# Kernel tuning notes

Hardware: AMD Instinct MI355X
Metric: run time of the kernel (lower is better)

## Reference

```python
import jax, jax.numpy as jnp
import numpy as np

N_NODES = 50000
N_EDGES = 1_600_000
T = 2
F_IN = 128
F_OUT = 128


def setup_inputs() -> dict:
    key = jax.random.key(0)
    k1, k2, k3, k4, k5, k6 = jax.random.split(key, 6)
    node_features = jax.random.normal(k1, (N_NODES, T, F_IN), dtype=jnp.float32)
    edge_weights = jax.random.uniform(k2, (T, N_EDGES), dtype=jnp.float32)
    src = jax.random.randint(k3, (N_EDGES,), 0, N_NODES, dtype=jnp.int32)
    dst = jax.random.randint(k4, (N_EDGES,), 0, N_NODES, dtype=jnp.int32)
    W = jax.random.normal(k5, (F_OUT, F_IN), dtype=jnp.float32) / np.sqrt(F_IN)
    b = jax.random.normal(k6, (F_OUT,), dtype=jnp.float32) * 0.01
    return {"node_features": node_features, "edge_weights": edge_weights,
            "src": src, "dst": dst, "W": W, "b": b}


def reference(node_features, edge_weights, src, dst, W, b):
    # DGL: graph.edata['e'] = edge_weights.t().unsqueeze(-1)  -> [E, T, 1]
    w = jnp.transpose(edge_weights)[:, :, None]          # [E, T, 1]
    # u_mul_e: gather src node features, scale by edge weight -> [E, T, F]
    msg = node_features[src] * w
    # sum aggregation at destination nodes -> [N, T, F]
    h = jax.ops.segment_sum(msg, dst, num_segments=node_features.shape[0])
    # Linear(in_features, out_features) with bias
    return jnp.einsum('ntf,of->nto', h, W) + b
```

## Files before the change

kernel.cpp:

```cpp
#include <hip/hip_runtime.h>
#include <hip/hip_bf16.h>
#include <hip/hip_fp16.h>


#define TBLOCK 256
#define CAP 64
#define NGRP 8
#define GSH 5
#define GSZ (1 << GSH)
#define NQ 1563
#define BCAP 224
#define APB 1536

typedef _Float16 half8 __attribute__((ext_vector_type(8)));
typedef float    f32x4 __attribute__((ext_vector_type(4)));
typedef float    float4_v __attribute__((ext_vector_type(4)));

__global__ void __launch_bounds__(TBLOCK)
prep_kernel(const float* __restrict__ W, _Float16* __restrict__ Wfrag,
            int* __restrict__ qcnt, int qtotal) {
    int i = blockIdx.x * TBLOCK + threadIdx.x;
    if (i < 128 * 128) {
        int j  = i & 7;
        int r  = (i >> 3) & 15;
        int q  = i >> 7;
        int kg = q & 3;
        int s  = (q >> 2) & 3;
        int c  = q >> 4;
        Wfrag[i] = (_Float16)W[(size_t)(c * 16 + r) * 128 + s * 32 + kg * 8 + j];
    }
    if (i < qtotal) qcnt[i] = 0;
}

__device__ __forceinline__ void do_append(
        const int* __restrict__ src, const int* __restrict__ dst,
        const float* __restrict__ ew, int* __restrict__ qcnt,
        unsigned long long* __restrict__ buckets, int E, int ablk) {
    const int g = ablk & (NGRP - 1);
    int* qc = qcnt + (size_t)g * NQ;
    unsigned long long* bk = buckets + (size_t)g * NQ * BCAP;

    const int idx = ablk * TBLOCK + (int)threadIdx.x;
    const int stride = APB * TBLOCK * 4;

    for (int e4 = idx * 4; e4 < E; e4 += stride) {
        if (e4 + 3 < E) {
            int4   d4  = *(const int4*)&dst[e4];
            int4   s4  = *(const int4*)&src[e4];
            float4 w04 = *(const float4*)&ew[e4];
            float4 w14 = *(const float4*)&ew[(size_t)E + e4];
            const int   dd[4] = {d4.x, d4.y, d4.z, d4.w};
            const int   ss[4] = {s4.x, s4.y, s4.z, s4.w};
            const float w0[4] = {w04.x, w04.y, w04.z, w04.w};
            const float w1[4] = {w14.x, w14.y, w14.z, w14.w};
            #pragma unroll
            for (int k = 0; k < 4; ++k) {
                int d = dd[k];
                int q = d >> GSH, dloc = d & (GSZ - 1);
                int pos = atomicAdd(&qc[q], 1);
                if (pos < BCAP) {
                    __half2 hw = __floats2half2_rn(w0[k], w1[k]);
                    bk[(size_t)q * BCAP + pos] =
                        (unsigned long long)(unsigned)(ss[k] | (dloc << 16)) |
                        ((unsigned long long)(*(unsigned*)&hw) << 32);
                }
            }
        } else {
            for (int e = e4; e < E; ++e) {
                int d = dst[e];
                int q = d >> GSH, dloc = d & (GSZ - 1);
                int pos = atomicAdd(&qc[q], 1);
                if (pos < BCAP) {
                    __half2 hw = __floats2half2_rn(ew[e], ew[(size_t)E + e]);
                    bk[(size_t)q * BCAP + pos] =
                        (unsigned long long)(unsigned)(src[e] | (dloc << 16)) |
                        ((unsigned long long)(*(unsigned*)&hw) << 32);
                }
            }
        }
    }
}

__device__ __forceinline__ void do_transform(
        const float* __restrict__ x, const _Float16* __restrict__ Wfrag,
        __half* __restrict__ y, int nrows, int blk) {
    const int tid = threadIdx.x;
    const int l   = tid & 63;
    const int wv  = tid >> 6;
    const int r15 = l & 15;
    const int kg  = l >> 4;
    const int row = blk * 64 + wv * 16 + r15;
    const bool ok = row < nrows;

    const float* xrow = x + (size_t)(ok ? row : 0) * 128;

    half8 xf[4];
    #pragma unroll
    for (int s = 0; s < 4; ++s) {
        float4 u0 = *(const float4*)&xrow[s * 32 + kg * 8];
        float4 u1 = *(const float4*)&xrow[s * 32 + kg * 8 + 4];
        half8 h;
        h[0] = (_Float16)u0.x; h[1] = (_Float16)u0.y;
        h[2] = (_Float16)u0.z; h[3] = (_Float16)u0.w;
        h[4] = (_Float16)u1.x; h[5] = (_Float16)u1.y;
        h[6] = (_Float16)u1.z; h[7] = (_Float16)u1.w;
        xf[s] = h;
    }

    f32x4 acc[8] = {};
    #pragma unroll
    for (int s = 0; s < 4; ++s) {
        #pragma unroll
        for (int c = 0; c < 8; ++c) {
            half8 wf = *(const half8*)&Wfrag[(size_t)(c * 16 + s * 4 + kg) * 128 + r15 * 8];
            acc[c] = __builtin_amdgcn_mfma_f32_16x16x32_f16(wf, xf[s], acc[c], 0, 0, 0);
        }
    }

    if (ok) {
        #pragma unroll
        for (int c = 0; c < 8; ++c) {
            __half2 h0 = __floats2half2_rn(acc[c][0], acc[c][1]);
            __half2 h1 = __floats2half2_rn(acc[c][2], acc[c][3]);
            uint2 pk;
            pk.x = *(unsigned*)&h0;
            pk.y = *(unsigned*)&h1;
            *(uint2*)&y[(size_t)row * 128 + c * 16 + kg * 4] = pk;
        }
    }
}

__global__ void __launch_bounds__(TBLOCK)
fused_kernel(const float* __restrict__ x, const _Float16* __restrict__ Wfrag,
             __half* __restrict__ y,
             const int* __restrict__ src, const int* __restrict__ dst,
             const float* __restrict__ ew, int* __restrict__ qcnt,
             unsigned long long* __restrict__ buckets,
             int nrows, int E) {
    if ((int)blockIdx.x < APB)
        do_append(src, dst, ew, qcnt, buckets, E, blockIdx.x);
    else
        do_transform(x, Wfrag, y, nrows, blockIdx.x - APB);
}

__global__ void __launch_bounds__(TBLOCK)
pull2_kernel(const __half* __restrict__ y, const int* __restrict__ qcnt,
             const unsigned long long* __restrict__ buckets,
             const float* __restrict__ b, float* __restrict__ out, int N) {
    __shared__ int lcnt[GSZ];
    __shared__ unsigned long long lent[GSZ * CAP];

    const int q = blockIdx.x;
    const int tid = threadIdx.x;
    if (tid < GSZ) lcnt[tid] = 0;
    __syncthreads();

    #pragma unroll 1
    for (int g = 0; g < NGRP; ++g) {
        int c = qcnt[(size_t)g * NQ + q];
        if (c > BCAP) c = BCAP;
        const unsigned long long* bk = buckets + ((size_t)g * NQ + q) * BCAP;
        for (int i = tid; i < c; i += TBLOCK) {
            unsigned long long ent = bk[i];
            int dloc = (int)((ent >> 16) & (GSZ - 1));
            int pos = atomicAdd(&lcnt[dloc], 1);
            if (pos < CAP) lent[dloc * CAP + pos] = ent;
        }
    }
    __syncthreads();

    const int wv   = __builtin_amdgcn_readfirstlane(tid >> 6);
    const int lane = tid & 63;
    const bool hi  = lane >= 32;
    const uint2* yv = (const uint2*)y;
    const float4 bv = ((const float4*)b)[lane & 31];

    #define ACCUM(ee, rr) do {                                            \
        unsigned wbits = (unsigned)((ee) >> 32);                          \
        __half2 w2 = *(__half2*)&wbits;                                   \
        float aw = __half2float(hi ? __high2half(w2) : __low2half(w2));   \
        float2 f0 = __half22float2(*(const __half2*)&(rr).x);             \
        float2 f1 = __half22float2(*(const __half2*)&(rr).y);             \
        acc.x += aw * f0.x; acc.y += aw * f0.y;                           \
        acc.z += aw * f1.x; acc.w += aw * f1.y; } while (0)

    #pragma unroll 1
    for (int j = 0; j < GSZ / 4; ++j) {
        const int n = wv * (GSZ / 4) + j;
        const int node = q * GSZ + n;
        if (node >= N) break;
        int c = lcnt[n];
        if (c > CAP) c = CAP;
        const unsigned long long* lp = &lent[n * CAP];
        float4 acc = bv;
        int i = 0;
        for (; i + 3 < c; i += 4) {
            unsigned long long e0 = lp[i], e1 = lp[i + 1];
            unsigned long long e2 = lp[i + 2], e3 = lp[i + 3];
            uint2 r0 = yv[(size_t)(e0 & 0xFFFFu) * 64 + lane];
            uint2 r1 = yv[(size_t)(e1 & 0xFFFFu) * 64 + lane];
            uint2 r2 = yv[(size_t)(e2 & 0xFFFFu) * 64 + lane];
            uint2 r3 = yv[(size_t)(e3 & 0xFFFFu) * 64 + lane];
            ACCUM(e0, r0); ACCUM(e1, r1); ACCUM(e2, r2); ACCUM(e3, r3);
        }
        for (; i < c; ++i) {
            unsigned long long e0 = lp[i];
            uint2 r0 = yv[(size_t)(e0 & 0xFFFFu) * 64 + lane];
            ACCUM(e0, r0);
        }
        float4_v av; av.x = acc.x; av.y = acc.y; av.z = acc.z; av.w = acc.w;
        __builtin_nontemporal_store(
            av, (float4_v*)&((float4*)out)[(size_t)node * 64 + lane]);
    }
}

extern "C" void kernel_launch(void* const* d_in, const int* in_sizes, int n_in,
                              void* d_out, int out_size, void* d_ws, size_t ws_size,
                              hipStream_t stream) {
    const float* x   = (const float*)d_in[0];
    const float* ew  = (const float*)d_in[1];
    const int*   src = (const int*)d_in[2];
    const int*   dst = (const int*)d_in[3];
    const float* W   = (const float*)d_in[4];
    const float* b   = (const float*)d_in[5];
    float* out = (float*)d_out;

    const int E     = in_sizes[2];
    const int nrows = in_sizes[0] / 128;
    const int N     = nrows / 2;

    char* w8 = (char*)d_ws;
    __half* y  = (__half*)w8;      w8 += (size_t)nrows * 128 * sizeof(__half);
    int* qcnt  = (int*)w8;         w8 += (size_t)NGRP * NQ * sizeof(int);
    _Float16* Wfrag = (_Float16*)w8;  w8 += 128 * 128 * sizeof(_Float16);
    w8 = (char*)(((uintptr_t)w8 + 15) & ~(uintptr_t)15);
    unsigned long long* buckets = (unsigned long long*)w8;

    prep_kernel<<<64, TBLOCK, 0, stream>>>(W, Wfrag, qcnt, NGRP * NQ);

    const int TT = (nrows + 63) / 64;
    fused_kernel<<<APB + TT, TBLOCK, 0, stream>>>(
        x, Wfrag, y, src, dst, ew, qcnt, buckets, nrows, E);

    pull2_kernel<<<NQ, TBLOCK, 0, stream>>>(y, qcnt, buckets, b, out, N);
}
```

Baseline: 230.1 us.

## Move linear transform after aggregation, fused into pull kernel via LDS MFMA

```diff
diff --git a/kernel.cpp b/kernel.cpp
--- a/kernel.cpp
+++ b/kernel.cpp
@@ -7,10 +7,11 @@
 #define CAP 64
 #define NGRP 8
 #define GSH 5
-#define GSZ (1 << GSH)
+#define GSZ 32
 #define NQ 1563
 #define BCAP 224
 #define APB 1536
+#define CASTB 1024
 
 typedef _Float16 half8 __attribute__((ext_vector_type(8)));
 typedef float    f32x4 __attribute__((ext_vector_type(4)));
@@ -81,74 +82,43 @@
     }
 }
 
-__device__ __forceinline__ void do_transform(
-        const float* __restrict__ x, const _Float16* __restrict__ Wfrag,
-        __half* __restrict__ y, int nrows, int blk) {
-    const int tid = threadIdx.x;
-    const int l   = tid & 63;
-    const int wv  = tid >> 6;
-    const int r15 = l & 15;
-    const int kg  = l >> 4;
-    const int row = blk * 64 + wv * 16 + r15;
-    const bool ok = row < nrows;
-
-    const float* xrow = x + (size_t)(ok ? row : 0) * 128;
-
-    half8 xf[4];
-    #pragma unroll
-    for (int s = 0; s < 4; ++s) {
-        float4 u0 = *(const float4*)&xrow[s * 32 + kg * 8];
-        float4 u1 = *(const float4*)&xrow[s * 32 + kg * 8 + 4];
+__device__ __forceinline__ void do_cast(
+        const float* __restrict__ x, __half* __restrict__ x16,
+        int total_chunks, int cblk) {
+    int idx = cblk * TBLOCK + (int)threadIdx.x;
+    const int stride = CASTB * TBLOCK;
+    for (int p = idx; p < total_chunks; p += stride) {
+        const float4* g = (const float4*)(x + (size_t)p * 8);
+        float4 u0 = g[0], u1 = g[1];
         half8 h;
         h[0] = (_Float16)u0.x; h[1] = (_Float16)u0.y;
         h[2] = (_Float16)u0.z; h[3] = (_Float16)u0.w;
         h[4] = (_Float16)u1.x; h[5] = (_Float16)u1.y;
         h[6] = (_Float16)u1.z; h[7] = (_Float16)u1.w;
-        xf[s] = h;
-    }
-
-    f32x4 acc[8] = {};
-    #pragma unroll
-    for (int s = 0; s < 4; ++s) {
-        #pragma unroll
-        for (int c = 0; c < 8; ++c) {
-            half8 wf = *(const half8*)&Wfrag[(size_t)(c * 16 + s * 4 + kg) * 128 + r15 * 8];
-            acc[c] = __builtin_amdgcn_mfma_f32_16x16x32_f16(wf, xf[s], acc[c], 0, 0, 0);
-        }
-    }
-
-    if (ok) {
-        #pragma unroll
-        for (int c = 0; c < 8; ++c) {
-            __half2 h0 = __floats2half2_rn(acc[c][0], acc[c][1]);
-            __half2 h1 = __floats2half2_rn(acc[c][2], acc[c][3]);
-            uint2 pk;
-            pk.x = *(unsigned*)&h0;
-            pk.y = *(unsigned*)&h1;
-            *(uint2*)&y[(size_t)row * 128 + c * 16 + kg * 4] = pk;
-        }
+        *(half8*)(x16 + (size_t)p * 8) = h;
     }
 }
 
 __global__ void __launch_bounds__(TBLOCK)
-fused_kernel(const float* __restrict__ x, const _Float16* __restrict__ Wfrag,
-             __half* __restrict__ y,
+fused_kernel(const float* __restrict__ x, __half* __restrict__ x16,
              const int* __restrict__ src, const int* __restrict__ dst,
              const float* __restrict__ ew, int* __restrict__ qcnt,
              unsigned long long* __restrict__ buckets,
-             int nrows, int E) {
+             int nchunks, int E) {
     if ((int)blockIdx.x < APB)
         do_append(src, dst, ew, qcnt, buckets, E, blockIdx.x);
     else
-        do_transform(x, Wfrag, y, nrows, blockIdx.x - APB);
+        do_cast(x, x16, nchunks, blockIdx.x - APB);
 }
 
 __global__ void __launch_bounds__(TBLOCK)
-pull2_kernel(const __half* __restrict__ y, const int* __restrict__ qcnt,
+pull3_kernel(const __half* __restrict__ x16, const int* __restrict__ qcnt,
              const unsigned long long* __restrict__ buckets,
-             const float* __restrict__ b, float* __restrict__ out, int N) {
+             const _Float16* __restrict__ Wfrag, const float* __restrict__ b,
+             float* __restrict__ out, int N) {
     __shared__ int lcnt[GSZ];
     __shared__ unsigned long long lent[GSZ * CAP];
+    __shared__ _Float16 hl[64 * 128];
 
     const int q = blockIdx.x;
     const int tid = threadIdx.x;
@@ -172,8 +142,7 @@
     const int wv   = __builtin_amdgcn_readfirstlane(tid >> 6);
     const int lane = tid & 63;
     const bool hi  = lane >= 32;
-    const uint2* yv = (const uint2*)y;
-    const float4 bv = ((const float4*)b)[lane & 31];
+    const uint2* yv = (const uint2*)x16;
 
     #define ACCUM(ee, rr) do {                                            \
         unsigned wbits = (unsigned)((ee) >> 32);                          \
@@ -192,7 +161,7 @@
         int c = lcnt[n];
         if (c > CAP) c = CAP;
         const unsigned long long* lp = &lent[n * CAP];
-        float4 acc = bv;
+        float4 acc = make_float4(0.f, 0.f, 0.f, 0.f);
         int i = 0;
         for (; i + 3 < c; i += 4) {
             unsigned long long e0 = lp[i], e1 = lp[i + 1];
@@ -208,9 +177,52 @@
             uint2 r0 = yv[(size_t)(e0 & 0xFFFFu) * 64 + lane];
             ACCUM(e0, r0);
         }
-        float4_v av; av.x = acc.x; av.y = acc.y; av.z = acc.z; av.w = acc.w;
-        __builtin_nontemporal_store(
-            av, (float4_v*)&((float4*)out)[(size_t)node * 64 + lane]);
+        int hrow = n * 2 + (hi ? 1 : 0);
+        int ch0  = (lane & 31) >> 1;
+        int sub  = (lane & 1) * 8;
+        __half2 p0 = __floats2half2_rn(acc.x, acc.y);
+        __half2 p1 = __floats2half2_rn(acc.z, acc.w);
+        uint2 pk;
+        pk.x = *(unsigned*)&p0;
+        pk.y = *(unsigned*)&p1;
+        *(uint2*)((char*)hl + hrow * 256 + ((ch0 ^ (hrow & 7)) << 4) + sub) = pk;
+    }
+    __syncthreads();
+
+    const int r15  = lane & 15;
+    const int kg   = lane >> 4;
+    const int rloc = wv * 16 + r15;
+
+    half8 xf[4];
+    #pragma unroll
+    for (int s = 0; s < 4; ++s) {
+        int chR = s * 4 + kg;
+        xf[s] = *(const half8*)((const char*)hl + rloc * 256 + ((chR ^ (rloc & 7)) << 4));
+    }
+
+    f32x4 acc2[8] = {};
+    #pragma unroll
+    for (int s = 0; s < 4; ++s) {
+        #pragma unroll
+        for (int c = 0; c < 8; ++c) {
+            half8 wf = *(const half8*)&Wfrag[(size_t)(c * 16 + s * 4 + kg) * 128 + r15 * 8];
+            acc2[c] = __builtin_amdgcn_mfma_f32_16x16x32_f16(wf, xf[s], acc2[c], 0, 0, 0);
+        }
+    }
+
+    const int gr = q * 64 + rloc;
+    if (gr < 2 * N) {
+        #pragma unroll
+        for (int c = 0; c < 8; ++c) {
+            float4 bb4 = *(const float4*)&b[c * 16 + kg * 4];
+            float4_v av;
+            av.x = acc2[c][0] + bb4.x;
+            av.y = acc2[c][1] + bb4.y;
+            av.z = acc2[c][2] + bb4.z;
+            av.w = acc2[c][3] + bb4.w;
+            __builtin_nontemporal_store(
+                av, (float4_v*)&out[(size_t)gr * 128 + c * 16 + kg * 4]);
+        }
     }
 }
 
@@ -230,17 +242,17 @@
     const int N     = nrows / 2;
 
     char* w8 = (char*)d_ws;
-    __half* y  = (__half*)w8;      w8 += (size_t)nrows * 128 * sizeof(__half);
-    int* qcnt  = (int*)w8;         w8 += (size_t)NGRP * NQ * sizeof(int);
+    __half* x16 = (__half*)w8;     w8 += (size_t)nrows * 128 * sizeof(__half);
+    int* qcnt   = (int*)w8;        w8 += (size_t)NGRP * NQ * sizeof(int);
     _Float16* Wfrag = (_Float16*)w8;  w8 += 128 * 128 * sizeof(_Float16);
     w8 = (char*)(((uintptr_t)w8 + 15) & ~(uintptr_t)15);
     unsigned long long* buckets = (unsigned long long*)w8;
 
     prep_kernel<<<64, TBLOCK, 0, stream>>>(W, Wfrag, qcnt, NGRP * NQ);
 
-    const int TT = (nrows + 63) / 64;
-    fused_kernel<<<APB + TT, TBLOCK, 0, stream>>>(
-        x, Wfrag, y, src, dst, ew, qcnt, buckets, nrows, E);
-
-    pull2_kernel<<<NQ, TBLOCK, 0, stream>>>(y, qcnt, buckets, b, out, N);
-}
+    const int nchunks = nrows * 16;
+    fused_kernel<<<APB + CASTB, TBLOCK, 0, stream>>>(
+        x, x16, src, dst, ew, qcnt, buckets, nchunks, E);
+
+    pull3_kernel<<<NQ, TBLOCK, 0, stream>>>(x16, qcnt, buckets, Wfrag, b, out, N);
+}
```

Measured after the change: 208.8 us, median of 2. 9.2% less time.
